# Optimization experiments

Measured on AMD Instinct MI355X. Metric: run time of the kernel, lower is better.

Reference implementation:

```python
import jax, jax.numpy as jnp
import numpy as np

NUM_CLASSES = 81
THRESHOLD = 0.5
NEGPOS_RATIO = 3
VARIANCE = (0.1, 0.2)


def point_form(p):
    # center-size -> corner form
    return jnp.concatenate([p[:, :2] - p[:, 2:] / 2, p[:, :2] + p[:, 2:] / 2], axis=1)


def jaccard(box_a, box_b):
    # box_a: [O,4] corners, box_b: [P,4] corners -> IoU [O,P]
    lt = jnp.maximum(box_a[:, None, :2], box_b[None, :, :2])
    rb = jnp.minimum(box_a[:, None, 2:], box_b[None, :, 2:])
    wh = jnp.clip(rb - lt, 0.0)
    inter = wh[..., 0] * wh[..., 1]
    area_a = ((box_a[:, 2] - box_a[:, 0]) * (box_a[:, 3] - box_a[:, 1]))[:, None]
    area_b = ((box_b[:, 2] - box_b[:, 0]) * (box_b[:, 3] - box_b[:, 1]))[None, :]
    return inter / (area_a + area_b - inter)


def encode(matched, priors, variances):
    # matched: [P,4] corner GT, priors: [P,4] center-size
    g_cxcy = (matched[:, :2] + matched[:, 2:]) / 2 - priors[:, :2]
    g_cxcy = g_cxcy / (variances[0] * priors[:, 2:])
    g_wh = (matched[:, 2:] - matched[:, :2]) / priors[:, 2:]
    g_wh = jnp.log(g_wh) / variances[1]
    return jnp.concatenate([g_cxcy, g_wh], axis=1)


def match_one(truths, labels, priors):
    overlaps = jaccard(truths, point_form(priors))   # [O,P]
    best_prior_idx = jnp.argmax(overlaps, axis=1)     # [O] best prior per truth
    best_truth_overlap = jnp.max(overlaps, axis=0)    # [P]
    best_truth_idx = jnp.argmax(overlaps, axis=0)     # [P] best truth per prior
    # force each truth's best prior to match that truth
    best_truth_overlap = best_truth_overlap.at[best_prior_idx].set(2.0)
    best_truth_idx = best_truth_idx.at[best_prior_idx].set(jnp.arange(truths.shape[0]))
    matched = truths[best_truth_idx]                  # [P,4]
    conf = labels[best_truth_idx].astype(jnp.int32) + 1
    conf = jnp.where(best_truth_overlap < THRESHOLD, 0, conf)
    loc = encode(matched, priors, VARIANCE)
    return loc, conf


def _loss(loc_data, conf_data, targets, priors):
    B, P, C = conf_data.shape
    loc_t, conf_t = jax.vmap(lambda t: match_one(t[:, :4], t[:, 4], priors))(targets)
    pos = conf_t > 0                                  # [B,P]
    # smooth-L1 (beta=1) over positive priors, sum reduction
    d = loc_data - loc_t
    sl1 = jnp.where(jnp.abs(d) < 1.0, 0.5 * d * d, jnp.abs(d) - 0.5)
    loss_l = jnp.sum(jnp.where(pos[..., None], sl1, 0.0))
    # per-prior CE used both for mining ranking and the final conf loss
    ce = jax.nn.logsumexp(conf_data, axis=-1) - jnp.take_along_axis(
        conf_data, conf_t[..., None], axis=-1)[..., 0]   # [B,P]
    # hard negative mining: zero positives, double argsort for rank
    loss_c_rank = jnp.where(pos, 0.0, ce)
    loss_idx = jnp.argsort(-loss_c_rank, axis=1)
    idx_rank = jnp.argsort(loss_idx, axis=1)
    num_pos = jnp.sum(pos, axis=1, keepdims=True)     # [B,1]
    num_neg = jnp.minimum(NEGPOS_RATIO * num_pos, P - 1)
    neg = idx_rank < num_neg
    sel = pos | neg
    loss_c = jnp.sum(jnp.where(sel, ce, 0.0))
    N = jnp.sum(num_pos).astype(loc_data.dtype)
    return loss_l / N, loss_c / N


def setup_inputs():
    key = jax.random.key(0)
    kl, kc, kb1, kb2, kll, kp1, kp2 = jax.random.split(key, 7)
    B, P, O, C = 64, 8732, 50, NUM_CLASSES
    loc_data = jax.random.normal(kl, (B, P, 4), jnp.float32)
    conf_data = jax.random.normal(kc, (B, P, C), jnp.float32)
    # valid GT boxes in corner form inside [0,1]
    cxcy = jax.random.uniform(kb1, (B, O, 2), minval=0.2, maxval=0.8)
    wh = jax.random.uniform(kb2, (B, O, 2), minval=0.05, maxval=0.3)
    boxes = jnp.concatenate([cxcy - wh / 2, cxcy + wh / 2], axis=-1)
    labels = jax.random.randint(kll, (B, O), 0, C - 1).astype(jnp.float32)
    targets = jnp.concatenate([boxes, labels[..., None]], axis=-1)  # [B,O,5]
    # priors in center-size form
    pcxcy = jax.random.uniform(kp1, (P, 2), minval=0.05, maxval=0.95)
    pwh = jax.random.uniform(kp2, (P, 2), minval=0.05, maxval=0.5)
    priors = jnp.concatenate([pcxcy, pwh], axis=-1)
    return {"loc_data": loc_data, "conf_data": conf_data, "targets": targets, "priors": priors}


def reference(loc_data, conf_data, targets, priors):
    return _loss(loc_data, conf_data, targets, priors)
```

## Files before the change

### kernel.cpp

```cpp
#include <hip/hip_runtime.h>
#include <float.h>

#pragma clang fp contract(off)

typedef unsigned long long ull;
typedef unsigned int u32;

#define THRESH 0.5f
#define PPT 4
#define CE_R 128
#define SEL_T 512
#define ENC_SEG 1024


__device__ __forceinline__ float sl1(float d) {
    float a = fabsf(d);
    return (a < 1.f) ? 0.5f * d * d : a - 0.5f;
}

__global__ __launch_bounds__(256) void k_prep(
        const float* __restrict__ targets, const float* __restrict__ priors,
        float* __restrict__ bto, int* __restrict__ bti, ull* __restrict__ tbest,
        u32* __restrict__ zws, int nz,
        int P, int O, int S, int SB, int npairs) {
    const int bid = blockIdx.x;
    __shared__ float4 tbox[128];
    __shared__ float tarea[128];
    if (bid < SB) {
        if (bid == 0)
            for (int i = threadIdx.x; i < nz; i += 256) zws[i] = 0;
        const int b = bid / S, seg = bid % S;
        const float* trow = targets + (size_t)b * O * 5;
        for (int o = threadIdx.x; o < O; o += 256) {
            float x1 = trow[o * 5 + 0], y1 = trow[o * 5 + 1];
            float x2 = trow[o * 5 + 2], y2 = trow[o * 5 + 3];
            tbox[o] = make_float4(x1, y1, x2, y2);
            tarea[o] = (x2 - x1) * (y2 - y1);
        }
        __syncthreads();
        const int p0 = seg * (256 * PPT);
        float px1[PPT], py1[PPT], px2[PPT], py2[PPT], pa[PPT];
        float bestv[PPT]; int besto[PPT]; int pidx[PPT];
#pragma unroll
        for (int j = 0; j < PPT; j++) {
            int p = p0 + (int)threadIdx.x + j * 256;
            pidx[j] = p; bestv[j] = -1.f; besto[j] = 0;
            if (p < P) {
                float4 pr = ((const float4*)priors)[p];
                px1[j] = pr.x - pr.z / 2.f;
                py1[j] = pr.y - pr.w / 2.f;
                px2[j] = pr.x + pr.z / 2.f;
                py2[j] = pr.y + pr.w / 2.f;
                pa[j] = (px2[j] - px1[j]) * (py2[j] - py1[j]);
            } else {
                px1[j] = 2.f; py1[j] = 2.f; px2[j] = 2.f; py2[j] = 2.f; pa[j] = 1.f;
            }
        }
        for (int o = 0; o < O; o++) {
            float4 t = tbox[o];
            float ta = tarea[o];
#pragma unroll
            for (int j = 0; j < PPT; j++) {
                float lx = fmaxf(t.x, px1[j]), ly = fmaxf(t.y, py1[j]);
                float rx = fminf(t.z, px2[j]), ry = fminf(t.w, py2[j]);
                float wx = fmaxf(rx - lx, 0.f), wy = fmaxf(ry - ly, 0.f);
                float inter = wx * wy;
                float iou = 0.f;
                if (inter > 0.f) iou = inter / (ta + pa[j] - inter);
                if (iou > bestv[j]) { bestv[j] = iou; besto[j] = o; }
            }
        }
#pragma unroll
        for (int j = 0; j < PPT; j++) {
            if (pidx[j] < P) {
                bto[(size_t)b * P + pidx[j]] = bestv[j];
                bti[(size_t)b * P + pidx[j]] = besto[j];
            }
        }
    } else {
        int g = (bid - SB) * 4 + ((int)threadIdx.x >> 6);
        int lane = threadIdx.x & 63;
        if (g >= npairs) return;
        int OP = (O + 1) >> 1;
        int b = g / OP;
        int o0 = (g % OP) * 2;
        const float* trow = targets + ((size_t)b * O + o0) * 5;
        float ax1 = trow[0], ay1 = trow[1], ax2 = trow[2], ay2 = trow[3];
        float ta0 = (ax2 - ax1) * (ay2 - ay1);
        bool has1 = (o0 + 1) < O;
        float cx1 = 0, cy1 = 0, cx2 = 0, cy2 = 0, ta1 = 1.f;
        if (has1) {
            cx1 = trow[5]; cy1 = trow[6]; cx2 = trow[7]; cy2 = trow[8];
            ta1 = (cx2 - cx1) * (cy2 - cy1);
        }
        ull k0 = 0, k1 = 0;
        for (int p = lane; p < P; p += 64) {
            float4 pr = ((const float4*)priors)[p];
            float bx1 = pr.x - pr.z / 2.f;
            float by1 = pr.y - pr.w / 2.f;
            float bx2 = pr.x + pr.z / 2.f;
            float by2 = pr.y + pr.w / 2.f;
            float pa = (bx2 - bx1) * (by2 - by1);
            u32 np = ~(u32)p;
            {
                float lx = fmaxf(ax1, bx1), ly = fmaxf(ay1, by1);
                float rx = fminf(ax2, bx2), ry = fminf(ay2, by2);
                float wx = fmaxf(rx - lx, 0.f), wy = fmaxf(ry - ly, 0.f);
                float inter = wx * wy;
                float iou = 0.f;
                if (inter > 0.f) iou = inter / (ta0 + pa - inter);
                ull key = ((ull)__float_as_uint(iou) << 32) | np;
                if (key > k0) k0 = key;
            }
            if (has1) {
                float lx = fmaxf(cx1, bx1), ly = fmaxf(cy1, by1);
                float rx = fminf(cx2, bx2), ry = fminf(cy2, by2);
                float wx = fmaxf(rx - lx, 0.f), wy = fmaxf(ry - ly, 0.f);
                float inter = wx * wy;
                float iou = 0.f;
                if (inter > 0.f) iou = inter / (ta1 + pa - inter);
                ull key = ((ull)__float_as_uint(iou) << 32) | np;
                if (key > k1) k1 = key;
            }
        }
        for (int off = 32; off; off >>= 1) {
            ull a = __shfl_xor(k0, off); if (a > k0) k0 = a;
            ull d = __shfl_xor(k1, off); if (d > k1) k1 = d;
        }
        if (lane == 0) {
            tbest[(size_t)b * O + o0] = k0;
            if (has1) tbest[(size_t)b * O + o0 + 1] = k1;
        }
    }
}

__global__ __launch_bounds__(256) void k_encode_ce(
        const float* __restrict__ targets, const float* __restrict__ priors,
        const float* __restrict__ loc_data, const float* __restrict__ conf,
        const ull* __restrict__ tbest,
        float* __restrict__ F,
        int* __restrict__ conf_t,
        int* __restrict__ num_pos, float* __restrict__ loss_l,
        int P, int O) {
    const int b = blockIdx.y, seg = blockIdx.x;
    __shared__ float tr[64 * 5];
    __shared__ int ov[ENC_SEG];
    __shared__ int ct[ENC_SEG];
    __shared__ float s[CE_R * 81];
    __shared__ float redf[4]; __shared__ int redi[4];
    const int p0 = seg * ENC_SEG;
    const int p1 = min(p0 + ENC_SEG, P);
    const int nprior = p1 - p0;
    const float* trow = targets + (size_t)b * O * 5;
    for (int i = threadIdx.x; i < O * 5; i += 256) tr[i] = trow[i];
    for (int i = threadIdx.x; i < nprior; i += 256) ov[i] = -1;
    __syncthreads();
    if ((int)threadIdx.x < O) {
        ull tb = tbest[(size_t)b * O + threadIdx.x];
        u32 p = ~(u32)(tb & 0xFFFFFFFFULL);
        if (p >= (u32)P) p = 0;
        if ((int)p >= p0 && (int)p < p1) atomicMax(&ov[p - p0], (int)threadIdx.x);
    }
    __syncthreads();
    float ll = 0.f; int cnt = 0;
    for (int p = p0 + (int)threadIdx.x; p < p1; p += 256) {
        size_t idx = (size_t)b * P + p;
        int o = conf_t[idx];
        int ovv = ov[p - p0];
        bool forced = ovv >= 0;
        if (forced) o = ovv;
        float ovl = F[idx];
        int cv = (!forced && ovl < THRESH) ? 0 : ((int)tr[o * 5 + 4] + 1);
        conf_t[idx] = cv;
        ct[p - p0] = cv;
        if (cv > 0) {
            cnt++;
            float4 pr = ((const float4*)priors)[p];
            float mx1 = tr[o * 5], my1 = tr[o * 5 + 1];
            float mx2 = tr[o * 5 + 2], my2 = tr[o * 5 + 3];
            float gx = ((mx1 + mx2) / 2.f - pr.x) / (0.1f * pr.z);
            float gy = ((my1 + my2) / 2.f - pr.y) / (0.1f * pr.w);
            float gw = logf((mx2 - mx1) / pr.z) / 0.2f;
            float gh = logf((my2 - my1) / pr.w) / 0.2f;
            float4 ld = ((const float4*)loc_data)[idx];
            ll += sl1(ld.x - gx) + sl1(ld.y - gy) + sl1(ld.z - gw) + sl1(ld.w - gh);
        }
    }
    for (int off = 32; off; off >>= 1) {
        ll += __shfl_down(ll, off);
        cnt += __shfl_down(cnt, off);
    }
    int w = threadIdx.x >> 6;
    if ((threadIdx.x & 63) == 0) { redf[w] = ll; redi[w] = cnt; }
    __syncthreads();
    if (threadIdx.x == 0) {
        float l = 0; int c = 0;
        for (int i = 0; i < 4; i++) { l += redf[i]; c += redi[i]; }
        if (c) atomicAdd(&num_pos[b], c);
        atomicAdd(&loss_l[b], l);
    }
    for (int c0 = 0; c0 < nprior; c0 += CE_R) {
        __syncthreads();
        int nrow = min(CE_R, nprior - c0);
        int nfl = nrow * 81;
        const float* src = conf + ((size_t)b * P + p0 + c0) * 81;
        int nv4 = nfl >> 2;
        for (int i = threadIdx.x; i < nv4; i += 256)
            ((float4*)s)[i] = ((const float4*)src)[i];
        for (int i = (nv4 << 2) + (int)threadIdx.x; i < nfl; i += 256)
            s[i] = src[i];
        __syncthreads();
        int row = threadIdx.x >> 1;
        int half = threadIdx.x & 1;
        if (row < nrow) {
            const float* rp = s + row * 81;
            int cc0 = half * 41;
            int cn = half ? 40 : 41;
            float sum = 0.f;
            for (int j = 0; j < cn; j++) sum += __expf(rp[cc0 + j]);
            sum += __shfl_xor(sum, 1);
            if (half == 0) {
                int t = ct[c0 + row];
                F[(size_t)b * P + p0 + c0 + row] = __logf(sum) - rp[t];
            }
        }
    }
}

__global__ __launch_bounds__(SEL_T) void k_select(
        const float* __restrict__ ce, const int* __restrict__ conf_t,
        const int* __restrict__ num_pos, const float* __restrict__ loss_l,
        float* __restrict__ acc, u32* __restrict__ ticket,
        float* __restrict__ out, int P, int B) {
    extern __shared__ u32 sk[];
    __shared__ u32 whist[SEL_T / 64][16];
    __shared__ u32 hist[16];
    __shared__ float redf[SEL_T / 64]; __shared__ u32 redu[SEL_T / 64];
    __shared__ u32 sh_pval; __shared__ int sh_rem;
    const int b = blockIdx.x;
    const size_t base = (size_t)b * P;
    const int lane = threadIdx.x & 63;
    const int w = threadIdx.x >> 6;
    const int NW = SEL_T / 64;

    float ps = 0.f;
    for (int p = threadIdx.x; p < P; p += SEL_T) {
        int c = conf_t[base + p];
        float v = ce[base + p];
        u32 key;
        if (c > 0) { ps += v; key = 0u; }
        else key = __float_as_uint(fmaxf(v, 0.f));
        sk[p] = key;
    }
    for (int off = 32; off; off >>= 1) ps += __shfl_down(ps, off);
    if (lane == 0) redf[w] = ps;
    __syncthreads();
    float pos_sum = 0.f;
    if (threadIdx.x == 0) {
        for (int i = 0; i < NW; i++) pos_sum += redf[i];
    }

    const int np = num_pos[b];
    const int k = min(3 * np, P - 1);
    u32 pval = 0, pmask = 0; int rem = k;
    if (k > 0) {
        for (int shift = 28; shift >= 0; shift -= 4) {
            __syncthreads();
            ull a0 = 0, a1 = 0;
            for (int p = threadIdx.x; p < P; p += SEL_T) {
                u32 key = sk[p];
                if ((key & pmask) == pval) {
                    u32 dig = (key >> shift) & 15u;
                    ull inc = 1ull << ((dig & 7u) * 8u);
                    if (dig < 8u) a0 += inc; else a1 += inc;
                }
            }
            const ull M = 0x00FF00FF00FF00FFull;
            ull e0 = a0 & M, e1 = (a0 >> 8) & M, e2 = a1 & M, e3 = (a1 >> 8) & M;
            for (int off = 32; off; off >>= 1) {
                e0 += __shfl_xor(e0, off);
                e1 += __shfl_xor(e1, off);
                e2 += __shfl_xor(e2, off);
                e3 += __shfl_xor(e3, off);
            }
            if (lane == 0) {
#pragma unroll
                for (int j = 0; j < 4; j++) {
                    whist[w][2 * j]     = (u32)((e0 >> (16 * j)) & 0xFFFF);
                    whist[w][2 * j + 1] = (u32)((e1 >> (16 * j)) & 0xFFFF);
                    whist[w][8 + 2 * j]     = (u32)((e2 >> (16 * j)) & 0xFFFF);
                    whist[w][8 + 2 * j + 1] = (u32)((e3 >> (16 * j)) & 0xFFFF);
                }
            }
            __syncthreads();
            if (threadIdx.x < 16) {
                u32 h = 0;
                for (int i = 0; i < NW; i++) h += whist[i][threadIdx.x];
                hist[threadIdx.x] = h;
            }
            __syncthreads();
            if (threadIdx.x == 0) {
                u32 accu = 0; int d = 15;
                for (; d > 0; d--) {
                    u32 h = hist[d];
                    if (accu + h >= (u32)rem) break;
                    accu += h;
                }
                sh_pval = pval | ((u32)d << shift);
                sh_rem = rem - (int)accu;
            }
            __syncthreads();
            pval = sh_pval; rem = sh_rem; pmask |= (0xFu << shift);
        }
    }

    float sgt = 0.f; u32 cgt = 0;
    if (k > 0) {
        for (int p = threadIdx.x; p < P; p += SEL_T) {
            u32 key = sk[p];
            if (key > pval) { sgt += __uint_as_float(key); cgt++; }
        }
    }
    for (int off = 32; off; off >>= 1) {
        sgt += __shfl_down(sgt, off);
        cgt += __shfl_down(cgt, off);
    }
    __syncthreads();
    if (lane == 0) { redf[w] = sgt; redu[w] = cgt; }
    __syncthreads();
    if (threadIdx.x == 0) {
        float s = 0.f; u32 c = 0;
        for (int i = 0; i < NW; i++) { s += redf[i]; c += redu[i]; }
        float t = __uint_as_float(pval);
        float lc_b = pos_sum + ((k > 0) ? (s + (float)(k - (int)c) * t) : 0.f);
        atomicAdd(&acc[0], (float)np);
        atomicAdd(&acc[1], loss_l[b]);
        atomicAdd(&acc[2], lc_b);
        __threadfence();
        u32 tk = atomicAdd(ticket, 1u);
        if (tk == (u32)(B - 1)) {
            float n  = atomicAdd(&acc[0], 0.f);
            float ll = atomicAdd(&acc[1], 0.f);
            float lc = atomicAdd(&acc[2], 0.f);
            out[0] = ll / n;
            out[1] = lc / n;
        }
    }
}


extern "C" void kernel_launch(void* const* d_in, const int* in_sizes, int n_in,
                              void* d_out, int out_size, void* d_ws, size_t ws_size,
                              hipStream_t stream) {
    const float* loc     = (const float*)d_in[0];
    const float* conf    = (const float*)d_in[1];
    const float* targets = (const float*)d_in[2];
    const float* priors  = (const float*)d_in[3];

    const int P = in_sizes[3] / 4;
    const int B = in_sizes[0] / (P * 4);
    const int O = in_sizes[2] / (B * 5);

    char* ws = (char*)d_ws;
    size_t off = 0;
    int*   num_pos = (int*)(ws + off);   off += (size_t)B * sizeof(int);
    float* loss_l  = (float*)(ws + off); off += (size_t)B * sizeof(float);
    float* acc     = (float*)(ws + off); off += 4 * sizeof(float);
    u32*   ticket  = (u32*)(ws + off);   off += sizeof(u32);
    const int zwords = (int)(off >> 2);
    off = (off + 7) & ~(size_t)7;
    ull*   tbest   = (ull*)(ws + off);   off += (size_t)B * O * sizeof(ull);
    float* F       = (float*)(ws + off); off += (size_t)B * P * sizeof(float);
    int*   I       = (int*)(ws + off);   off += (size_t)B * P * sizeof(int);

    const int SEG = 256 * PPT;
    const int S = (P + SEG - 1) / SEG;
    const int SB = S * B;
    const int npairs = B * ((O + 1) / 2);
    const int TB = (npairs + 3) / 4;
    k_prep<<<SB + TB, 256, 0, stream>>>(targets, priors, F, I, tbest,
                                        (u32*)ws, zwords, P, O, S, SB, npairs);

    const int S2 = (P + ENC_SEG - 1) / ENC_SEG;
    k_encode_ce<<<dim3(S2, B), 256, 0, stream>>>(targets, priors, loc, conf, tbest,
                                                 F, I, num_pos, loss_l, P, O);

    k_select<<<B, SEL_T, (size_t)P * sizeof(u32), stream>>>(F, I, num_pos, loss_l,
                                                            acc, ticket, (float*)d_out, P, B);
}
```

Measured before the change: 386.8 us.

## Move log-sum-exp computation into prep kernel, gather target logit later

The per-prior log-sum-exp over the 81 class logits moves out of the encode kernel into extra blocks of the prep kernel. These blocks run alongside the IoU matching blocks because they do not depend on the matching result. The encode kernel then only gathers one target logit per prior and subtracts it from the stored LSE, which removes the staged confidence tile in shared memory. In exchange it adds a B*P float buffer that is written and read again, plus one scattered gather into the confidence tensor per prior. It also makes the prep kernel larger and raises its shared memory use.

```diff
diff --git a/kernel.cpp b/kernel.cpp
--- a/kernel.cpp
+++ b/kernel.cpp
@@ -20,16 +20,42 @@
 
 __global__ __launch_bounds__(256) void k_prep(
         const float* __restrict__ targets, const float* __restrict__ priors,
+        const float* __restrict__ conf,
         float* __restrict__ bto, int* __restrict__ bti, ull* __restrict__ tbest,
+        float* __restrict__ lse,
         u32* __restrict__ zws, int nz,
-        int P, int O, int S, int SB, int npairs) {
+        int P, int O, int S, int CB, int SB, int npairs, long long BP) {
     const int bid = blockIdx.x;
     __shared__ float4 tbox[128];
     __shared__ float tarea[128];
-    if (bid < SB) {
+    __shared__ float s[CE_R * 81];
+    if (bid < CB) {
         if (bid == 0)
             for (int i = threadIdx.x; i < nz; i += 256) zws[i] = 0;
-        const int b = bid / S, seg = bid % S;
+        long long r0 = (long long)bid * CE_R;
+        int nrow = (int)min((long long)CE_R, BP - r0);
+        int nfl = nrow * 81;
+        const float* src = conf + r0 * 81;
+        int nv4 = nfl >> 2;
+        for (int i = threadIdx.x; i < nv4; i += 256)
+            ((float4*)s)[i] = ((const float4*)src)[i];
+        for (int i = (nv4 << 2) + (int)threadIdx.x; i < nfl; i += 256)
+            s[i] = src[i];
+        __syncthreads();
+        int row = threadIdx.x >> 1;
+        int half = threadIdx.x & 1;
+        if (row < nrow) {
+            const float* rp = s + row * 81;
+            int c0 = half * 41;
+            int cn = half ? 40 : 41;
+            float sum = 0.f;
+            for (int j = 0; j < cn; j++) sum += __expf(rp[c0 + j]);
+            sum += __shfl_xor(sum, 1);
+            if (half == 0) lse[r0 + row] = __logf(sum);
+        }
+    } else if (bid < CB + SB) {
+        const int ab = bid - CB;
+        const int b = ab / S, seg = ab % S;
         const float* trow = targets + (size_t)b * O * 5;
         for (int o = threadIdx.x; o < O; o += 256) {
             float x1 = trow[o * 5 + 0], y1 = trow[o * 5 + 1];
@@ -78,7 +104,7 @@
             }
         }
     } else {
-        int g = (bid - SB) * 4 + ((int)threadIdx.x >> 6);
+        int g = (bid - CB - SB) * 4 + ((int)threadIdx.x >> 6);
         int lane = threadIdx.x & 63;
         if (g >= npairs) return;
         int OP = (O + 1) >> 1;
@@ -137,7 +163,7 @@
 __global__ __launch_bounds__(256) void k_encode_ce(
         const float* __restrict__ targets, const float* __restrict__ priors,
         const float* __restrict__ loc_data, const float* __restrict__ conf,
-        const ull* __restrict__ tbest,
+        const ull* __restrict__ tbest, const float* __restrict__ lse,
         float* __restrict__ F,
         int* __restrict__ conf_t,
         int* __restrict__ num_pos, float* __restrict__ loss_l,
@@ -145,8 +171,6 @@
     const int b = blockIdx.y, seg = blockIdx.x;
     __shared__ float tr[64 * 5];
     __shared__ int ov[ENC_SEG];
-    __shared__ int ct[ENC_SEG];
-    __shared__ float s[CE_R * 81];
     __shared__ float redf[4]; __shared__ int redi[4];
     const int p0 = seg * ENC_SEG;
     const int p1 = min(p0 + ENC_SEG, P);
@@ -172,7 +196,6 @@
         float ovl = F[idx];
         int cv = (!forced && ovl < THRESH) ? 0 : ((int)tr[o * 5 + 4] + 1);
         conf_t[idx] = cv;
-        ct[p - p0] = cv;
         if (cv > 0) {
             cnt++;
             float4 pr = ((const float4*)priors)[p];
@@ -185,6 +208,8 @@
             float4 ld = ((const float4*)loc_data)[idx];
             ll += sl1(ld.x - gx) + sl1(ld.y - gy) + sl1(ld.z - gw) + sl1(ld.w - gh);
         }
+        float tv = conf[idx * 81 + cv];
+        F[idx] = lse[idx] - tv;
     }
     for (int off = 32; off; off >>= 1) {
         ll += __shfl_down(ll, off);
@@ -198,32 +223,6 @@
         for (int i = 0; i < 4; i++) { l += redf[i]; c += redi[i]; }
         if (c) atomicAdd(&num_pos[b], c);
         atomicAdd(&loss_l[b], l);
-    }
-    for (int c0 = 0; c0 < nprior; c0 += CE_R) {
-        __syncthreads();
-        int nrow = min(CE_R, nprior - c0);
-        int nfl = nrow * 81;
-        const float* src = conf + ((size_t)b * P + p0 + c0) * 81;
-        int nv4 = nfl >> 2;
-        for (int i = threadIdx.x; i < nv4; i += 256)
-            ((float4*)s)[i] = ((const float4*)src)[i];
-        for (int i = (nv4 << 2) + (int)threadIdx.x; i < nfl; i += 256)
-            s[i] = src[i];
-        __syncthreads();
-        int row = threadIdx.x >> 1;
-        int half = threadIdx.x & 1;
-        if (row < nrow) {
-            const float* rp = s + row * 81;
-            int cc0 = half * 41;
-            int cn = half ? 40 : 41;
-            float sum = 0.f;
-            for (int j = 0; j < cn; j++) sum += __expf(rp[cc0 + j]);
-            sum += __shfl_xor(sum, 1);
-            if (half == 0) {
-                int t = ct[c0 + row];
-                F[(size_t)b * P + p0 + c0 + row] = __logf(sum) - rp[t];
-            }
-        }
     }
 }
 
@@ -360,6 +359,7 @@
     const int P = in_sizes[3] / 4;
     const int B = in_sizes[0] / (P * 4);
     const int O = in_sizes[2] / (B * 5);
+    const long long BP = (long long)B * P;
 
     char* ws = (char*)d_ws;
     size_t off = 0;
@@ -370,19 +370,21 @@
     const int zwords = (int)(off >> 2);
     off = (off + 7) & ~(size_t)7;
     ull*   tbest   = (ull*)(ws + off);   off += (size_t)B * O * sizeof(ull);
-    float* F       = (float*)(ws + off); off += (size_t)B * P * sizeof(float);
-    int*   I       = (int*)(ws + off);   off += (size_t)B * P * sizeof(int);
+    float* F       = (float*)(ws + off); off += (size_t)BP * sizeof(float);
+    int*   I       = (int*)(ws + off);   off += (size_t)BP * sizeof(int);
+    float* L       = (float*)(ws + off); off += (size_t)BP * sizeof(float);
 
     const int SEG = 256 * PPT;
     const int S = (P + SEG - 1) / SEG;
     const int SB = S * B;
     const int npairs = B * ((O + 1) / 2);
     const int TB = (npairs + 3) / 4;
-    k_prep<<<SB + TB, 256, 0, stream>>>(targets, priors, F, I, tbest,
-                                        (u32*)ws, zwords, P, O, S, SB, npairs);
+    const int CB = (int)((BP + CE_R - 1) / CE_R);
+    k_prep<<<CB + SB + TB, 256, 0, stream>>>(targets, priors, conf, F, I, tbest, L,
+                                             (u32*)ws, zwords, P, O, S, CB, SB, npairs, BP);
 
     const int S2 = (P + ENC_SEG - 1) / ENC_SEG;
-    k_encode_ce<<<dim3(S2, B), 256, 0, stream>>>(targets, priors, loc, conf, tbest,
+    k_encode_ce<<<dim3(S2, B), 256, 0, stream>>>(targets, priors, loc, conf, tbest, L,
                                                  F, I, num_pos, loss_l, P, O);
 
     k_select<<<B, SEL_T, (size_t)P * sizeof(u32), stream>>>(F, I, num_pos, loss_l,
```

New measurement: 390.6 us. Within noise of the previous version (+1.0%).
